# Kernel optimization log

Measured on AMD Instinct MI355X. Metric: run time of the kernel, lower is better.

Reference implementation:

```python
import jax, jax.numpy as jnp
import numpy as np

LR_X = 0.1  # learning_rates[0] from init_kwargs
N_SENSORY = 784


def setup_inputs() -> dict:
    key = jax.random.key(0)
    k1, k2 = jax.random.split(key, 2)
    B, N = 256, 4096
    x = jax.random.normal(k1, (B, N), dtype=jnp.float32)
    # w initialized small, as in _reset_params (0.0001 fill + 1e-4 noise, masked by adj)
    w = jax.random.normal(k2, (N, N), dtype=jnp.float32) * 0.01
    # 1 = node whose value is updated (internal + supervised), 0 = clamped sensory node
    update_mask = jnp.concatenate(
        [jnp.zeros(N_SENSORY, jnp.int32), jnp.ones(N - N_SENSORY, jnp.int32)])
    return {"x": x, "w": w, "update_mask": update_mask, "T": 32}


def reference(x, w, update_mask, T):
    # vanZwol_AMB iterative predictive-coding inference, f = tanh
    m = update_mask.astype(x.dtype)  # [N], 1 = free node

    def f(v):
        return jnp.tanh(v)

    def dfdx(v):
        return 1.0 - jnp.tanh(v) ** 2

    def step(xs, _):
        mu = f(xs) @ w.T                      # [B,N] prediction
        e = (xs - mu) * m                     # use_input_error=False: zero sensory errors
        dEdx = e - dfdx(xs) * (e @ w)         # grad_x (vanZwol_AMB)
        xs = xs - LR_X * m * dEdx             # only internal/supervised nodes updated
        return xs, None

    x, _ = jax.lax.scan(step, x, None, length=T)
    return x
```

## Files before the change

kernel.cpp:

```cpp
#include <hip/hip_runtime.h>
#include <stdint.h>
#include <stddef.h>


#define N_DIM 4096
#define B_DIM 256
#define T_STEPS 32
#define LR_X 0.1f
#define N0 768
#define N_LIVE 3328
#define NCHL 52
#define KG 4
#define KITG 13

typedef unsigned short ushort_t;
using bf16x8 = __attribute__((ext_vector_type(8))) __bf16;
using f32x4  = __attribute__((ext_vector_type(4))) float;

__device__ __forceinline__ ushort_t f2bf(float f) {
    union { float f; unsigned int u; } v; v.f = f;
    unsigned int r = v.u + 0x7fffu + ((v.u >> 16) & 1u);
    return (ushort_t)(r >> 16);
}
__device__ __forceinline__ float bf2f(ushort_t h) {
    union { unsigned int u; float f; } v; v.u = ((unsigned int)h) << 16;
    return v.f;
}

__device__ __forceinline__ int pkidx(int r, int c) {
    const int s = ((r >> 4) << 1) | ((c >> 5) & 1);
    return s * 512 + (r & 15) * 8 + (((c >> 3) & 3) << 7) + (c & 7);
}

__device__ __forceinline__ void async_copy16(const ushort_t* g, ushort_t* l) {
    __builtin_amdgcn_global_load_lds(
        (__attribute__((address_space(1))) void*)(g),
        (__attribute__((address_space(3))) void*)(l),
        16, 0, 0);
}

__global__ __launch_bounds__(256) void pack_w(const float* __restrict__ w,
                                              ushort_t* __restrict__ wpk,
                                              ushort_t* __restrict__ wtpk) {
    __shared__ float tile[64][68];
    const int tid = threadIdx.x;
    const int bid = blockIdx.x;
    int row0, col0; ushort_t* dst; bool tr;
    if (bid < 52 * 64) {
        tr   = false;
        dst  = wpk + (size_t)bid * 4096;
        row0 = N0 + (bid >> 6) * 64;
        col0 = (bid & 63) * 64;
    } else {
        const int b2 = bid - 52 * 64;
        tr   = true;
        dst  = wtpk + (size_t)b2 * 4096;
        const int ntile = b2 / 52, chunk = b2 - ntile * 52;
        row0 = N0 + chunk * 64;
        col0 = N0 + ntile * 64;
    }
    const int rr = tid >> 2, c0 = (tid & 3) * 16;
    const float* src = w + (size_t)(row0 + rr) * N_DIM + col0 + c0;
#pragma unroll
    for (int i = 0; i < 16; i += 4)
        *(float4*)&tile[rr][c0 + i] = *(const float4*)(src + i);
    __syncthreads();
    ushort_t loc[16];
#pragma unroll
    for (int i = 0; i < 16; ++i) {
        const int p = tid * 16 + i;
        const int s = p >> 9, e = p & 511;
        const int r = ((s >> 1) << 4) | ((e >> 3) & 15);
        const int c = ((s & 1) << 5) | (((e >> 7) & 3) << 3) | (e & 7);
        loc[i] = f2bf(tr ? tile[c][r] : tile[r][c]);
    }
    *(uint4*)&dst[tid * 16]     = *(uint4*)&loc[0];
    *(uint4*)&dst[tid * 16 + 8] = *(uint4*)&loc[8];
}

__global__ __launch_bounds__(256) void pack_t_init(const float* __restrict__ xin,
                                                   float* __restrict__ xout,
                                                   ushort_t* __restrict__ tpk) {
    __shared__ float tile[64][68];
    const int tid  = threadIdx.x;
    const int bid  = blockIdx.x;
    const int row0 = (bid >> 6) * 64;
    const int col0 = (bid & 63) * 64;
    const int rr = tid >> 2, c0 = (tid & 3) * 16;
    const size_t sidx = (size_t)(row0 + rr) * N_DIM + col0 + c0;
#pragma unroll
    for (int i = 0; i < 16; i += 4) {
        float4 v = *(const float4*)(xin + sidx + i);
        *(float4*)(xout + sidx + i) = v;
        tile[rr][c0 + i + 0] = tanhf(v.x);
        tile[rr][c0 + i + 1] = tanhf(v.y);
        tile[rr][c0 + i + 2] = tanhf(v.z);
        tile[rr][c0 + i + 3] = tanhf(v.w);
    }
    __syncthreads();
    ushort_t loc[16];
    ushort_t* dst = tpk + (size_t)bid * 4096;
#pragma unroll
    for (int i = 0; i < 16; ++i) {
        const int p = tid * 16 + i;
        const int s = p >> 9, e = p & 511;
        const int r = ((s >> 1) << 4) | ((e >> 3) & 15);
        const int c = ((s & 1) << 5) | (((e >> 7) & 3) << 3) | (e & 7);
        loc[i] = f2bf(tile[r][c]);
    }
    *(uint4*)&dst[tid * 16]     = *(uint4*)&loc[0];
    *(uint4*)&dst[tid * 16 + 8] = *(uint4*)&loc[8];
}

__global__ __launch_bounds__(256) void gemm_mu0(const ushort_t* __restrict__ Apk,
                                                const ushort_t* __restrict__ Bpk,
                                                float* __restrict__ mu0) {
    __shared__ __align__(16) ushort_t As[2][4096];
    __shared__ __align__(16) ushort_t Bs[2][4096];
    const int tid  = threadIdx.x;
    const int lane = tid & 63;
    const int wid  = tid >> 6;
    const int wave_m = wid >> 1, wave_n = wid & 1;
    const int ntile = blockIdx.x, mtile = blockIdx.y;

    const ushort_t* Ab = Apk + (size_t)mtile * 64 * 4096;
    const ushort_t* Bb = Bpk + (size_t)ntile * 64 * 4096;

    auto stage = [&](int buf, int kt) {
#pragma unroll
        for (int u = 0; u < 2; ++u) {
            const int off = (wid * 2 + u) * 512 + lane * 8;
            async_copy16(Ab + (size_t)kt * 4096 + off, &As[buf][off]);
            async_copy16(Bb + (size_t)kt * 4096 + off, &Bs[buf][off]);
        }
    };
    f32x4 acc[2][2] = {};
    auto compute = [&](int buf) {
#pragma unroll
        for (int ks = 0; ks < 2; ++ks) {
            bf16x8 a[2], b[2];
#pragma unroll
            for (int i = 0; i < 2; ++i) {
                const int asub = (wave_m * 2 + i) * 2 + ks;
                const int bsub = (wave_n * 2 + i) * 2 + ks;
                a[i] = *(const bf16x8*)(&As[buf][asub * 512 + lane * 8]);
                b[i] = *(const bf16x8*)(&Bs[buf][bsub * 512 + lane * 8]);
            }
#pragma unroll
            for (int i = 0; i < 2; ++i)
#pragma unroll
                for (int j = 0; j < 2; ++j)
                    acc[i][j] = __builtin_amdgcn_mfma_f32_16x16x32_bf16(
                        a[i], b[j], acc[i][j], 0, 0, 0);
        }
    };
    stage(0, 0);
    __syncthreads();
    for (int kt = 0; kt < 12; ++kt) {
        if (kt + 1 < 12) stage((kt + 1) & 1, kt + 1);
        compute(kt & 1);
        __syncthreads();
    }
    const int l15 = lane & 15, quad = lane >> 4;
#pragma unroll
    for (int j = 0; j < 2; ++j) {
        const int nl = ntile * 64 + wave_n * 32 + j * 16 + l15;
#pragma unroll
        for (int i = 0; i < 2; ++i)
#pragma unroll
            for (int r = 0; r < 4; ++r) {
                const int m = mtile * 64 + wave_m * 32 + i * 16 + quad * 4 + r;
                mu0[(size_t)m * N_LIVE + nl] = acc[i][j][r];
            }
    }
}

template <int SA, int SB, int CO, int PHASE>
__global__ __launch_bounds__(1024) void gemm_fused(
    const ushort_t* __restrict__ Apk,
    const ushort_t* __restrict__ Bpk,
    float* __restrict__ xbuf,
    const float* __restrict__ mu0,
    const int* __restrict__ mask,
    ushort_t* __restrict__ epk,
    ushort_t* __restrict__ tpk) {
    __shared__ __align__(16) ushort_t smem[65536];
    ushort_t* As = smem;
    ushort_t* Bs = smem + 32768;

    const int bid = blockIdx.x;
    const int xcd = bid & 7;
    const int i   = bid >> 3;
    const int nloc = (xcd < 4) ? 7 : 6;
    if (i >= nloc * 4) return;
    const int n0    = (xcd < 4) ? xcd * 7 : 28 + (xcd - 4) * 6;
    const int ntile = n0 + (i >> 2);
    const int mtile = i & 3;

    const int tid  = threadIdx.x;
    const int lane = tid & 63;
    const int g    = tid >> 8;
    const int gtid = tid & 255;
    const int gw   = (tid >> 6) & 3;
    const int wave_m = gw >> 1, wave_n = gw & 1;

    const ushort_t* Ab = Apk + ((size_t)mtile * SA + CO + g * KITG) * 4096;
    const ushort_t* Bb = Bpk + ((size_t)ntile * SB + CO + g * KITG) * 4096;

    auto stage = [&](int buf, int kt) {
        const ushort_t* Ac = Ab + (size_t)kt * 4096;
        const ushort_t* Bc = Bb + (size_t)kt * 4096;
#pragma unroll
        for (int u = 0; u < 2; ++u) {
            const int off = (u * 256 + gtid) * 8;
            async_copy16(Ac + off, &As[(g * 2 + buf) * 4096 + off]);
            async_copy16(Bc + off, &Bs[(g * 2 + buf) * 4096 + off]);
        }
    };

    f32x4 acc[2][2] = {};

    auto compute = [&](int buf) {
#pragma unroll
        for (int ks = 0; ks < 2; ++ks) {
            bf16x8 a[2], b[2];
#pragma unroll
            for (int i2 = 0; i2 < 2; ++i2) {
                const int asub = (wave_m * 2 + i2) * 2 + ks;
                const int bsub = (wave_n * 2 + i2) * 2 + ks;
                a[i2] = *(const bf16x8*)(&As[(g * 2 + buf) * 4096 + asub * 512 + lane * 8]);
                b[i2] = *(const bf16x8*)(&Bs[(g * 2 + buf) * 4096 + bsub * 512 + lane * 8]);
            }
#pragma unroll
            for (int i2 = 0; i2 < 2; ++i2)
#pragma unroll
                for (int j = 0; j < 2; ++j)
                    acc[i2][j] = __builtin_amdgcn_mfma_f32_16x16x32_bf16(
                        a[i2], b[j], acc[i2][j], 0, 0, 0);
        }
    };

    stage(0, 0);
    for (int kt = 0; kt < KITG; ++kt) {
        if (kt + 1 < KITG) {
            stage((kt + 1) & 1, kt + 1);
            asm volatile("s_waitcnt vmcnt(4)" ::: "memory");
        } else {
            asm volatile("s_waitcnt vmcnt(0)" ::: "memory");
        }
        __builtin_amdgcn_s_barrier();
        __builtin_amdgcn_sched_barrier(0);
        compute(kt & 1);
        __builtin_amdgcn_s_barrier();
    }
    __syncthreads();

    float* red = (float*)smem;
    const int RP = 64 * 68;
    {
        const int l15 = lane & 15, quad = lane >> 4;
#pragma unroll
        for (int j = 0; j < 2; ++j) {
            const int col = wave_n * 32 + j * 16 + l15;
#pragma unroll
            for (int i2 = 0; i2 < 2; ++i2)
#pragma unroll
                for (int r = 0; r < 4; ++r) {
                    const int row = wave_m * 32 + i2 * 16 + quad * 4 + r;
                    red[g * RP + row * 68 + col] = acc[i2][j][r];
                }
        }
    }
    __syncthreads();

    const int p4 = tid * 4;
    const int s  = p4 >> 9, e9 = p4 & 511;
    const int r  = ((s >> 1) << 4) | ((e9 >> 3) & 15);
    const int c  = ((s & 1) << 5) | (((e9 >> 7) & 3) << 3) | (e9 & 7);

    float4 sv = *(const float4*)&red[0 * RP + r * 68 + c];
#pragma unroll
    for (int gg = 1; gg < KG; ++gg) {
        float4 v = *(const float4*)&red[gg * RP + r * 68 + c];
        sv.x += v.x; sv.y += v.y; sv.z += v.z; sv.w += v.w;
    }

    const int grow = mtile * 64 + r;
    const int gcl  = ntile * 64 + c;
    const size_t xi = (size_t)grow * N_DIM + N0 + gcl;
    float4 xv = *(const float4*)&xbuf[xi];
    int4   mk = *(const int4*)&mask[N0 + gcl];

    if (PHASE == 1) {
        float4 m0 = *(const float4*)&mu0[(size_t)grow * N_LIVE + gcl];
        ushort_t ev[4];
        ev[0] = f2bf((xv.x - (m0.x + sv.x)) * (float)mk.x);
        ev[1] = f2bf((xv.y - (m0.y + sv.y)) * (float)mk.y);
        ev[2] = f2bf((xv.z - (m0.z + sv.z)) * (float)mk.z);
        ev[3] = f2bf((xv.w - (m0.w + sv.w)) * (float)mk.w);
        *(uint2*)&epk[((size_t)(mtile * NCHL + ntile)) * 4096 + p4]
            = *(uint2*)&ev[0];
    } else {
        const ushort_t* ech = Apk + ((size_t)(mtile * SA + ntile)) * 4096;
        ushort_t ein[4];
        *(uint2*)&ein[0] = *(const uint2*)&ech[p4];
        float xn[4]; ushort_t tv[4];
        const float* svp = &sv.x;
        const int*   mkp = &mk.x;
        const float* xvp = &xv.x;
#pragma unroll
        for (int q = 0; q < 4; ++q) {
            const float x  = xvp[q];
            const float th = tanhf(x);
            const float ee = bf2f(ein[q]);
            xn[q] = x - LR_X * (float)mkp[q] * (ee - (1.0f - th * th) * svp[q]);
            tv[q] = f2bf(tanhf(xn[q]));
        }
        *(float4*)&xbuf[xi] = make_float4(xn[0], xn[1], xn[2], xn[3]);
        *(uint2*)&tpk[((size_t)(mtile * 64 + 12 + ntile)) * 4096 + p4]
            = *(uint2*)&tv[0];
    }
}

extern "C" void kernel_launch(void* const* d_in, const int* in_sizes, int n_in,
                              void* d_out, int out_size, void* d_ws, size_t ws_size,
                              hipStream_t stream) {
    const float* x_in  = (const float*)d_in[0];
    const float* w_in  = (const float*)d_in[1];
    const int*   mask  = (const int*)d_in[2];
    float*       xbuf  = (float*)d_out;

    uint8_t* ws = (uint8_t*)d_ws;
    ushort_t* w_pk  = (ushort_t*)(ws);
    ushort_t* wt_pk = (ushort_t*)(ws + 27262976);
    ushort_t* t_pk  = (ushort_t*)(ws + 49414144);
    ushort_t* e_pk  = (ushort_t*)(ws + 51511296);
    float*    mu0   = (float*)(ws + 53215232);

    pack_w<<<dim3(52 * 64 + 52 * 52), 256, 0, stream>>>(w_in, w_pk, wt_pk);
    pack_t_init<<<dim3(4 * 64), 256, 0, stream>>>(x_in, xbuf, t_pk);
    gemm_mu0<<<dim3(52, 4), 256, 0, stream>>>(t_pk, w_pk, mu0);

    for (int t = 0; t < T_STEPS; ++t) {
        gemm_fused<64, 64, 12, 1><<<256, 1024, 0, stream>>>(
            t_pk, w_pk, xbuf, mu0, mask, e_pk, t_pk);
        gemm_fused<52, 52, 0, 2><<<256, 1024, 0, stream>>>(
            e_pk, wt_pk, xbuf, mu0, mask, e_pk, t_pk);
    }
}
```

Baseline: 1.032 ms.

## Fuse all time steps into one persistent kernel with grid barriers

Replaces the 64 per-step kernel launches with a single persistent kernel that loops over all T steps and synchronises the 208 active blocks with an atomic grid barrier between the two GEMM phases. Each block keeps its x tile, mask and mu0 values in registers across steps, and reuses the fp32 error instead of reloading the bf16 copy. This removes launch gaps and repeated global loads, but relies on all blocks being co-resident and adds spin-wait barrier latency.

```diff
diff --git a/kernel.cpp b/kernel.cpp
--- a/kernel.cpp
+++ b/kernel.cpp
@@ -12,6 +12,7 @@
 #define NCHL 52
 #define KG 4
 #define KITG 13
+#define NB_ACTIVE 208
 
 typedef unsigned short ushort_t;
 using bf16x8 = __attribute__((ext_vector_type(8))) __bf16;
@@ -25,11 +26,6 @@
 __device__ __forceinline__ float bf2f(ushort_t h) {
     union { unsigned int u; float f; } v; v.u = ((unsigned int)h) << 16;
     return v.f;
-}
-
-__device__ __forceinline__ int pkidx(int r, int c) {
-    const int s = ((r >> 4) << 1) | ((c >> 5) & 1);
-    return s * 512 + (r & 15) * 8 + (((c >> 3) & 3) << 7) + (c & 7);
 }
 
 __device__ __forceinline__ void async_copy16(const ushort_t* g, ushort_t* l) {
@@ -175,15 +171,40 @@
     }
 }
 
-template <int SA, int SB, int CO, int PHASE>
-__global__ __launch_bounds__(1024) void gemm_fused(
-    const ushort_t* __restrict__ Apk,
-    const ushort_t* __restrict__ Bpk,
+__global__ void bar_init(unsigned* bar) { bar[0] = 0u; bar[1] = 0u; }
+
+__device__ __forceinline__ void grid_bar(unsigned* bar) {
+    __syncthreads();
+    if (threadIdx.x == 0) {
+        __threadfence();
+        unsigned g = __hip_atomic_load(&bar[1], __ATOMIC_RELAXED,
+                                       __HIP_MEMORY_SCOPE_AGENT);
+        unsigned v = __hip_atomic_fetch_add(&bar[0], 1u, __ATOMIC_ACQ_REL,
+                                            __HIP_MEMORY_SCOPE_AGENT);
+        if (v == NB_ACTIVE - 1) {
+            __hip_atomic_store(&bar[0], 0u, __ATOMIC_RELAXED,
+                               __HIP_MEMORY_SCOPE_AGENT);
+            __hip_atomic_fetch_add(&bar[1], 1u, __ATOMIC_RELEASE,
+                                   __HIP_MEMORY_SCOPE_AGENT);
+        } else {
+            while (__hip_atomic_load(&bar[1], __ATOMIC_ACQUIRE,
+                                     __HIP_MEMORY_SCOPE_AGENT) == g)
+                __builtin_amdgcn_s_sleep(2);
+        }
+        __threadfence();
+    }
+    __syncthreads();
+}
+
+__global__ __launch_bounds__(1024) void pc_persist(
+    const ushort_t* __restrict__ w_pk,
+    const ushort_t* __restrict__ wt_pk,
+    ushort_t* __restrict__ t_pk,
+    ushort_t* __restrict__ e_pk,
     float* __restrict__ xbuf,
     const float* __restrict__ mu0,
     const int* __restrict__ mask,
-    ushort_t* __restrict__ epk,
-    ushort_t* __restrict__ tpk) {
+    unsigned* __restrict__ bar) {
     __shared__ __align__(16) ushort_t smem[65536];
     ushort_t* As = smem;
     ushort_t* Bs = smem + 32768;
@@ -203,62 +224,75 @@
     const int gtid = tid & 255;
     const int gw   = (tid >> 6) & 3;
     const int wave_m = gw >> 1, wave_n = gw & 1;
-
-    const ushort_t* Ab = Apk + ((size_t)mtile * SA + CO + g * KITG) * 4096;
-    const ushort_t* Bb = Bpk + ((size_t)ntile * SB + CO + g * KITG) * 4096;
-
-    auto stage = [&](int buf, int kt) {
-        const ushort_t* Ac = Ab + (size_t)kt * 4096;
-        const ushort_t* Bc = Bb + (size_t)kt * 4096;
-#pragma unroll
-        for (int u = 0; u < 2; ++u) {
-            const int off = (u * 256 + gtid) * 8;
-            async_copy16(Ac + off, &As[(g * 2 + buf) * 4096 + off]);
-            async_copy16(Bc + off, &Bs[(g * 2 + buf) * 4096 + off]);
-        }
-    };
-
-    f32x4 acc[2][2] = {};
-
-    auto compute = [&](int buf) {
-#pragma unroll
-        for (int ks = 0; ks < 2; ++ks) {
-            bf16x8 a[2], b[2];
-#pragma unroll
-            for (int i2 = 0; i2 < 2; ++i2) {
-                const int asub = (wave_m * 2 + i2) * 2 + ks;
-                const int bsub = (wave_n * 2 + i2) * 2 + ks;
-                a[i2] = *(const bf16x8*)(&As[(g * 2 + buf) * 4096 + asub * 512 + lane * 8]);
-                b[i2] = *(const bf16x8*)(&Bs[(g * 2 + buf) * 4096 + bsub * 512 + lane * 8]);
-            }
-#pragma unroll
-            for (int i2 = 0; i2 < 2; ++i2)
-#pragma unroll
-                for (int j = 0; j < 2; ++j)
-                    acc[i2][j] = __builtin_amdgcn_mfma_f32_16x16x32_bf16(
-                        a[i2], b[j], acc[i2][j], 0, 0, 0);
-        }
-    };
-
-    stage(0, 0);
-    for (int kt = 0; kt < KITG; ++kt) {
-        if (kt + 1 < KITG) {
-            stage((kt + 1) & 1, kt + 1);
-            asm volatile("s_waitcnt vmcnt(4)" ::: "memory");
-        } else {
-            asm volatile("s_waitcnt vmcnt(0)" ::: "memory");
-        }
-        __builtin_amdgcn_s_barrier();
-        __builtin_amdgcn_sched_barrier(0);
-        compute(kt & 1);
-        __builtin_amdgcn_s_barrier();
-    }
-    __syncthreads();
+    const int l15 = lane & 15, quad = lane >> 4;
+
+    ushort_t* Asg = As + g * 2 * 4096;
+    ushort_t* Bsg = Bs + g * 2 * 4096;
+
+    const int p4 = tid * 4;
+    const int s  = p4 >> 9, e9 = p4 & 511;
+    const int rr = ((s >> 1) << 4) | ((e9 >> 3) & 15);
+    const int cc = ((s & 1) << 5) | (((e9 >> 7) & 3) << 3) | (e9 & 7);
+    const int grow = mtile * 64 + rr;
+    const int gcl  = ntile * 64 + cc;
+    const size_t xi = (size_t)grow * N_DIM + N0 + gcl;
 
     float* red = (float*)smem;
     const int RP = 64 * 68;
-    {
-        const int l15 = lane & 15, quad = lane >> 4;
+
+    float4 xv = *(const float4*)&xbuf[xi];
+    const int4   mk = *(const int4*)&mask[N0 + gcl];
+    const float4 m0 = *(const float4*)&mu0[(size_t)grow * N_LIVE + gcl];
+    float em[4];
+
+    auto run_panel = [&](const ushort_t* Ab, const ushort_t* Bb,
+                         f32x4 (&acc)[2][2]) {
+        auto stage = [&](int buf, int kt) {
+            const ushort_t* Ac = Ab + (size_t)kt * 4096;
+            const ushort_t* Bc = Bb + (size_t)kt * 4096;
+#pragma unroll
+            for (int u = 0; u < 2; ++u) {
+                const int off = (u * 256 + gtid) * 8;
+                async_copy16(Ac + off, &Asg[buf * 4096 + off]);
+                async_copy16(Bc + off, &Bsg[buf * 4096 + off]);
+            }
+        };
+        auto compute = [&](int buf) {
+#pragma unroll
+            for (int ks = 0; ks < 2; ++ks) {
+                bf16x8 a[2], b[2];
+#pragma unroll
+                for (int i2 = 0; i2 < 2; ++i2) {
+                    const int asub = (wave_m * 2 + i2) * 2 + ks;
+                    const int bsub = (wave_n * 2 + i2) * 2 + ks;
+                    a[i2] = *(const bf16x8*)(&Asg[buf * 4096 + asub * 512 + lane * 8]);
+                    b[i2] = *(const bf16x8*)(&Bsg[buf * 4096 + bsub * 512 + lane * 8]);
+                }
+#pragma unroll
+                for (int i2 = 0; i2 < 2; ++i2)
+#pragma unroll
+                    for (int j = 0; j < 2; ++j)
+                        acc[i2][j] = __builtin_amdgcn_mfma_f32_16x16x32_bf16(
+                            a[i2], b[j], acc[i2][j], 0, 0, 0);
+            }
+        };
+        stage(0, 0);
+        for (int kt = 0; kt < KITG; ++kt) {
+            if (kt + 1 < KITG) {
+                stage((kt + 1) & 1, kt + 1);
+                asm volatile("s_waitcnt vmcnt(4)" ::: "memory");
+            } else {
+                asm volatile("s_waitcnt vmcnt(0)" ::: "memory");
+            }
+            __builtin_amdgcn_s_barrier();
+            __builtin_amdgcn_sched_barrier(0);
+            compute(kt & 1);
+            __builtin_amdgcn_s_barrier();
+        }
+    };
+
+    auto reduce_sum = [&](f32x4 (&acc)[2][2]) -> float4 {
+        __syncthreads();
 #pragma unroll
         for (int j = 0; j < 2; ++j) {
             const int col = wave_n * 32 + j * 16 + l15;
@@ -270,56 +304,57 @@
                     red[g * RP + row * 68 + col] = acc[i2][j][r];
                 }
         }
-    }
-    __syncthreads();
-
-    const int p4 = tid * 4;
-    const int s  = p4 >> 9, e9 = p4 & 511;
-    const int r  = ((s >> 1) << 4) | ((e9 >> 3) & 15);
-    const int c  = ((s & 1) << 5) | (((e9 >> 7) & 3) << 3) | (e9 & 7);
-
-    float4 sv = *(const float4*)&red[0 * RP + r * 68 + c];
-#pragma unroll
-    for (int gg = 1; gg < KG; ++gg) {
-        float4 v = *(const float4*)&red[gg * RP + r * 68 + c];
-        sv.x += v.x; sv.y += v.y; sv.z += v.z; sv.w += v.w;
-    }
-
-    const int grow = mtile * 64 + r;
-    const int gcl  = ntile * 64 + c;
-    const size_t xi = (size_t)grow * N_DIM + N0 + gcl;
-    float4 xv = *(const float4*)&xbuf[xi];
-    int4   mk = *(const int4*)&mask[N0 + gcl];
-
-    if (PHASE == 1) {
-        float4 m0 = *(const float4*)&mu0[(size_t)grow * N_LIVE + gcl];
-        ushort_t ev[4];
-        ev[0] = f2bf((xv.x - (m0.x + sv.x)) * (float)mk.x);
-        ev[1] = f2bf((xv.y - (m0.y + sv.y)) * (float)mk.y);
-        ev[2] = f2bf((xv.z - (m0.z + sv.z)) * (float)mk.z);
-        ev[3] = f2bf((xv.w - (m0.w + sv.w)) * (float)mk.w);
-        *(uint2*)&epk[((size_t)(mtile * NCHL + ntile)) * 4096 + p4]
-            = *(uint2*)&ev[0];
-    } else {
-        const ushort_t* ech = Apk + ((size_t)(mtile * SA + ntile)) * 4096;
-        ushort_t ein[4];
-        *(uint2*)&ein[0] = *(const uint2*)&ech[p4];
-        float xn[4]; ushort_t tv[4];
-        const float* svp = &sv.x;
-        const int*   mkp = &mk.x;
-        const float* xvp = &xv.x;
-#pragma unroll
-        for (int q = 0; q < 4; ++q) {
-            const float x  = xvp[q];
-            const float th = tanhf(x);
-            const float ee = bf2f(ein[q]);
-            xn[q] = x - LR_X * (float)mkp[q] * (ee - (1.0f - th * th) * svp[q]);
-            tv[q] = f2bf(tanhf(xn[q]));
-        }
-        *(float4*)&xbuf[xi] = make_float4(xn[0], xn[1], xn[2], xn[3]);
-        *(uint2*)&tpk[((size_t)(mtile * 64 + 12 + ntile)) * 4096 + p4]
-            = *(uint2*)&tv[0];
-    }
+        __syncthreads();
+        float4 sv = *(const float4*)&red[0 * RP + rr * 68 + cc];
+#pragma unroll
+        for (int gg = 1; gg < KG; ++gg) {
+            float4 v = *(const float4*)&red[gg * RP + rr * 68 + cc];
+            sv.x += v.x; sv.y += v.y; sv.z += v.z; sv.w += v.w;
+        }
+        return sv;
+    };
+
+    const ushort_t* Ab1 = t_pk + ((size_t)(mtile * 64 + 12 + g * KITG)) * 4096;
+    const ushort_t* Bb1 = w_pk + ((size_t)(ntile * 64 + 12 + g * KITG)) * 4096;
+    const ushort_t* Ab2 = e_pk + ((size_t)(mtile * NCHL + g * KITG)) * 4096;
+    const ushort_t* Bb2 = wt_pk + ((size_t)(ntile * NCHL + g * KITG)) * 4096;
+    ushort_t* eout = e_pk + ((size_t)(mtile * NCHL + ntile)) * 4096 + p4;
+    ushort_t* tout = t_pk + ((size_t)(mtile * 64 + 12 + ntile)) * 4096 + p4;
+
+    for (int t = 0; t < T_STEPS; ++t) {
+        {
+            f32x4 acc[2][2] = {};
+            run_panel(Ab1, Bb1, acc);
+            float4 sv = reduce_sum(acc);
+            em[0] = (xv.x - (m0.x + sv.x)) * (float)mk.x;
+            em[1] = (xv.y - (m0.y + sv.y)) * (float)mk.y;
+            em[2] = (xv.z - (m0.z + sv.z)) * (float)mk.z;
+            em[3] = (xv.w - (m0.w + sv.w)) * (float)mk.w;
+            ushort_t ev[4] = { f2bf(em[0]), f2bf(em[1]), f2bf(em[2]), f2bf(em[3]) };
+            *(uint2*)eout = *(uint2*)&ev[0];
+        }
+        grid_bar(bar);
+        {
+            f32x4 acc[2][2] = {};
+            run_panel(Ab2, Bb2, acc);
+            float4 sv = reduce_sum(acc);
+            float* xp = &xv.x;
+            const float* svp = &sv.x;
+            const int* mkp = &mk.x;
+            ushort_t tv[4];
+#pragma unroll
+            for (int q = 0; q < 4; ++q) {
+                const float x  = xp[q];
+                const float th = tanhf(x);
+                xp[q] = x - LR_X * (float)mkp[q]
+                            * (em[q] - (1.0f - th * th) * svp[q]);
+                tv[q] = f2bf(tanhf(xp[q]));
+            }
+            *(uint2*)tout = *(uint2*)&tv[0];
+        }
+        grid_bar(bar);
+    }
+    *(float4*)&xbuf[xi] = xv;
 }
 
 extern "C" void kernel_launch(void* const* d_in, const int* in_sizes, int n_in,
@@ -336,15 +371,13 @@
     ushort_t* t_pk  = (ushort_t*)(ws + 49414144);
     ushort_t* e_pk  = (ushort_t*)(ws + 51511296);
     float*    mu0   = (float*)(ws + 53215232);
+    unsigned* bar   = (unsigned*)(ws + 56623104);
 
     pack_w<<<dim3(52 * 64 + 52 * 52), 256, 0, stream>>>(w_in, w_pk, wt_pk);
     pack_t_init<<<dim3(4 * 64), 256, 0, stream>>>(x_in, xbuf, t_pk);
     gemm_mu0<<<dim3(52, 4), 256, 0, stream>>>(t_pk, w_pk, mu0);
-
-    for (int t = 0; t < T_STEPS; ++t) {
-        gemm_fused<64, 64, 12, 1><<<256, 1024, 0, stream>>>(
-            t_pk, w_pk, xbuf, mu0, mask, e_pk, t_pk);
-        gemm_fused<52, 52, 0, 2><<<256, 1024, 0, stream>>>(
-            e_pk, wt_pk, xbuf, mu0, mask, e_pk, t_pk);
-    }
-}
+    bar_init<<<1, 1, 0, stream>>>(bar);
+
+    pc_persist<<<256, 1024, 0, stream>>>(
+        w_pk, wt_pk, t_pk, e_pk, xbuf, mu0, mask, bar);
+}
```

Measured after the change: 3.447 ms. 234% more time.

## Store live weight blocks as scaled FP8 e4m3 and expand to bf16 in-kernel

Applied to the files above, without the earlier changes.

Packs the live-node weight blocks (both W and W^T) into FP8 e4m3 with a fixed scale of 256, keeping only the sensory columns in bf16 for the initial mu0 GEMM. The per-step fused GEMMs stream half as many weight bytes and convert FP8 to bf16 with bit manipulation before the bf16 MFMA. This targets the memory traffic of re-reading the weight matrix each iteration. It adds ALU work for conversion and loses precision, and the fixed scale assumes small-magnitude weights.

```diff
diff --git a/kernel.cpp b/kernel.cpp
--- a/kernel.cpp
+++ b/kernel.cpp
@@ -27,37 +27,68 @@
     return v.f;
 }
 
-__device__ __forceinline__ int pkidx(int r, int c) {
-    const int s = ((r >> 4) << 1) | ((c >> 5) & 1);
-    return s * 512 + (r & 15) * 8 + (((c >> 3) & 3) << 7) + (c & 7);
-}
-
-__device__ __forceinline__ void async_copy16(const ushort_t* g, ushort_t* l) {
+__device__ __forceinline__ unsigned char f2e4m3_s8(float f) {
+    f *= 256.0f;
+    union { float f; unsigned int u; } v; v.f = f;
+    const unsigned s = (v.u >> 24) & 0x80u;
+    const unsigned absu = v.u & 0x7FFFFFFFu;
+    const unsigned r = absu + 0x7FFFFu + ((absu >> 20) & 1u);
+    const int e4 = (int)((r >> 23) & 0xFF) - 120;
+    const unsigned m3 = (r >> 20) & 7u;
+    if (e4 <= 0)  return (unsigned char)s;
+    if (e4 > 15)  return (unsigned char)(s | 0x7E);
+    return (unsigned char)(s | ((unsigned)e4 << 3) | m3);
+}
+
+__device__ __forceinline__ bf16x8 fp8x8_to_bf16x8(uint2 d) {
+    union { unsigned u[4]; bf16x8 v; } o;
+    unsigned x = d.x;
+    o.u[0] = ((((x & 0x80u) << 8) | ((x & 0x8000u) << 16)
+             | ((x & 0x7Fu) << 4) | ((x & 0x7F00u) << 12)) + 0x38003800u);
+    x >>= 16;
+    o.u[1] = ((((x & 0x80u) << 8) | ((x & 0x8000u) << 16)
+             | ((x & 0x7Fu) << 4) | ((x & 0x7F00u) << 12)) + 0x38003800u);
+    unsigned y = d.y;
+    o.u[2] = ((((y & 0x80u) << 8) | ((y & 0x8000u) << 16)
+             | ((y & 0x7Fu) << 4) | ((y & 0x7F00u) << 12)) + 0x38003800u);
+    y >>= 16;
+    o.u[3] = ((((y & 0x80u) << 8) | ((y & 0x8000u) << 16)
+             | ((y & 0x7Fu) << 4) | ((y & 0x7F00u) << 12)) + 0x38003800u);
+    return o.v;
+}
+
+__device__ __forceinline__ void async_copy16(const void* g, void* l) {
     __builtin_amdgcn_global_load_lds(
-        (__attribute__((address_space(1))) void*)(g),
+        (__attribute__((address_space(1))) const void*)(g),
         (__attribute__((address_space(3))) void*)(l),
         16, 0, 0);
 }
 
 __global__ __launch_bounds__(256) void pack_w(const float* __restrict__ w,
-                                              ushort_t* __restrict__ wpk,
-                                              ushort_t* __restrict__ wtpk) {
+                                              ushort_t* __restrict__ wsen,
+                                              uint8_t* __restrict__ wl8,
+                                              uint8_t* __restrict__ wt8) {
     __shared__ float tile[64][68];
     const int tid = threadIdx.x;
     const int bid = blockIdx.x;
-    int row0, col0; ushort_t* dst; bool tr;
-    if (bid < 52 * 64) {
-        tr   = false;
-        dst  = wpk + (size_t)bid * 4096;
-        row0 = N0 + (bid >> 6) * 64;
-        col0 = (bid & 63) * 64;
+    int row0, col0; bool tr, f8; ushort_t* dst16 = nullptr; uint8_t* dst8 = nullptr;
+    if (bid < 624) {
+        tr = false; f8 = false;
+        const int ntile = bid / 12, ch = bid - ntile * 12;
+        row0 = N0 + ntile * 64; col0 = ch * 64;
+        dst16 = wsen + (size_t)bid * 4096;
+    } else if (bid < 3328) {
+        tr = false; f8 = true;
+        const int b2 = bid - 624;
+        const int ntile = b2 / 52, cl = b2 - ntile * 52;
+        row0 = N0 + ntile * 64; col0 = N0 + cl * 64;
+        dst8 = wl8 + (size_t)b2 * 4096;
     } else {
-        const int b2 = bid - 52 * 64;
-        tr   = true;
-        dst  = wtpk + (size_t)b2 * 4096;
-        const int ntile = b2 / 52, chunk = b2 - ntile * 52;
-        row0 = N0 + chunk * 64;
-        col0 = N0 + ntile * 64;
+        tr = true; f8 = true;
+        const int b3 = bid - 3328;
+        const int ntile = b3 / 52, cl = b3 - ntile * 52;
+        row0 = N0 + cl * 64; col0 = N0 + ntile * 64;
+        dst8 = wt8 + (size_t)b3 * 4096;
     }
     const int rr = tid >> 2, c0 = (tid & 3) * 16;
     const float* src = w + (size_t)(row0 + rr) * N_DIM + col0 + c0;
@@ -65,17 +96,30 @@
     for (int i = 0; i < 16; i += 4)
         *(float4*)&tile[rr][c0 + i] = *(const float4*)(src + i);
     __syncthreads();
-    ushort_t loc[16];
-#pragma unroll
-    for (int i = 0; i < 16; ++i) {
-        const int p = tid * 16 + i;
-        const int s = p >> 9, e = p & 511;
-        const int r = ((s >> 1) << 4) | ((e >> 3) & 15);
-        const int c = ((s & 1) << 5) | (((e >> 7) & 3) << 3) | (e & 7);
-        loc[i] = f2bf(tr ? tile[c][r] : tile[r][c]);
-    }
-    *(uint4*)&dst[tid * 16]     = *(uint4*)&loc[0];
-    *(uint4*)&dst[tid * 16 + 8] = *(uint4*)&loc[8];
+    if (!f8) {
+        ushort_t loc[16];
+#pragma unroll
+        for (int i = 0; i < 16; ++i) {
+            const int p = tid * 16 + i;
+            const int s = p >> 9, e = p & 511;
+            const int r = ((s >> 1) << 4) | ((e >> 3) & 15);
+            const int c = ((s & 1) << 5) | (((e >> 7) & 3) << 3) | (e & 7);
+            loc[i] = f2bf(tile[r][c]);
+        }
+        *(uint4*)&dst16[tid * 16]     = *(uint4*)&loc[0];
+        *(uint4*)&dst16[tid * 16 + 8] = *(uint4*)&loc[8];
+    } else {
+        unsigned char loc[16];
+#pragma unroll
+        for (int i = 0; i < 16; ++i) {
+            const int p = tid * 16 + i;
+            const int s = p >> 9, e = p & 511;
+            const int r = ((s >> 1) << 4) | ((e >> 3) & 15);
+            const int c = ((s & 1) << 5) | (((e >> 7) & 3) << 3) | (e & 7);
+            loc[i] = f2e4m3_s8(tr ? tile[c][r] : tile[r][c]);
+        }
+        *(uint4*)&dst8[tid * 16] = *(uint4*)&loc[0];
+    }
 }
 
 __global__ __launch_bounds__(256) void pack_t_init(const float* __restrict__ xin,
@@ -113,7 +157,7 @@
 }
 
 __global__ __launch_bounds__(256) void gemm_mu0(const ushort_t* __restrict__ Apk,
-                                                const ushort_t* __restrict__ Bpk,
+                                                const ushort_t* __restrict__ wsen,
                                                 float* __restrict__ mu0) {
     __shared__ __align__(16) ushort_t As[2][4096];
     __shared__ __align__(16) ushort_t Bs[2][4096];
@@ -124,7 +168,7 @@
     const int ntile = blockIdx.x, mtile = blockIdx.y;
 
     const ushort_t* Ab = Apk + (size_t)mtile * 64 * 4096;
-    const ushort_t* Bb = Bpk + (size_t)ntile * 64 * 4096;
+    const ushort_t* Bb = wsen + (size_t)ntile * 12 * 4096;
 
     auto stage = [&](int buf, int kt) {
 #pragma unroll
@@ -175,18 +219,18 @@
     }
 }
 
-template <int SA, int SB, int CO, int PHASE>
+template <int SA, int CO, int PHASE>
 __global__ __launch_bounds__(1024) void gemm_fused(
     const ushort_t* __restrict__ Apk,
-    const ushort_t* __restrict__ Bpk,
+    const uint8_t* __restrict__ Bpk8,
     float* __restrict__ xbuf,
     const float* __restrict__ mu0,
     const int* __restrict__ mask,
     ushort_t* __restrict__ epk,
     ushort_t* __restrict__ tpk) {
-    __shared__ __align__(16) ushort_t smem[65536];
-    ushort_t* As = smem;
-    ushort_t* Bs = smem + 32768;
+    __shared__ __align__(16) uint8_t smem[98304];
+    ushort_t* As  = (ushort_t*)smem;
+    uint8_t*  Bs8 = smem + 65536;
 
     const int bid = blockIdx.x;
     const int xcd = bid & 7;
@@ -205,17 +249,20 @@
     const int wave_m = gw >> 1, wave_n = gw & 1;
 
     const ushort_t* Ab = Apk + ((size_t)mtile * SA + CO + g * KITG) * 4096;
-    const ushort_t* Bb = Bpk + ((size_t)ntile * SB + CO + g * KITG) * 4096;
+    const uint8_t*  Bb = Bpk8 + ((size_t)ntile * NCHL + g * KITG) * 4096;
+
+    ushort_t* Asg = As + g * 2 * 4096;
+    uint8_t*  Bsg = Bs8 + g * 2 * 4096;
 
     auto stage = [&](int buf, int kt) {
         const ushort_t* Ac = Ab + (size_t)kt * 4096;
-        const ushort_t* Bc = Bb + (size_t)kt * 4096;
+        const uint8_t*  Bc = Bb + (size_t)kt * 4096;
 #pragma unroll
         for (int u = 0; u < 2; ++u) {
             const int off = (u * 256 + gtid) * 8;
-            async_copy16(Ac + off, &As[(g * 2 + buf) * 4096 + off]);
-            async_copy16(Bc + off, &Bs[(g * 2 + buf) * 4096 + off]);
-        }
+            async_copy16(Ac + off, &Asg[buf * 4096 + off]);
+        }
+        async_copy16(Bc + gtid * 16, &Bsg[buf * 4096 + gtid * 16]);
     };
 
     f32x4 acc[2][2] = {};
@@ -228,8 +275,9 @@
             for (int i2 = 0; i2 < 2; ++i2) {
                 const int asub = (wave_m * 2 + i2) * 2 + ks;
                 const int bsub = (wave_n * 2 + i2) * 2 + ks;
-                a[i2] = *(const bf16x8*)(&As[(g * 2 + buf) * 4096 + asub * 512 + lane * 8]);
-                b[i2] = *(const bf16x8*)(&Bs[(g * 2 + buf) * 4096 + bsub * 512 + lane * 8]);
+                a[i2] = *(const bf16x8*)(&Asg[buf * 4096 + asub * 512 + lane * 8]);
+                b[i2] = fp8x8_to_bf16x8(
+                    *(const uint2*)(&Bsg[buf * 4096 + bsub * 512 + lane * 8]));
             }
 #pragma unroll
             for (int i2 = 0; i2 < 2; ++i2)
@@ -244,7 +292,7 @@
     for (int kt = 0; kt < KITG; ++kt) {
         if (kt + 1 < KITG) {
             stage((kt + 1) & 1, kt + 1);
-            asm volatile("s_waitcnt vmcnt(4)" ::: "memory");
+            asm volatile("s_waitcnt vmcnt(3)" ::: "memory");
         } else {
             asm volatile("s_waitcnt vmcnt(0)" ::: "memory");
         }
@@ -331,20 +379,21 @@
     float*       xbuf  = (float*)d_out;
 
     uint8_t* ws = (uint8_t*)d_ws;
-    ushort_t* w_pk  = (ushort_t*)(ws);
-    ushort_t* wt_pk = (ushort_t*)(ws + 27262976);
-    ushort_t* t_pk  = (ushort_t*)(ws + 49414144);
-    ushort_t* e_pk  = (ushort_t*)(ws + 51511296);
-    float*    mu0   = (float*)(ws + 53215232);
-
-    pack_w<<<dim3(52 * 64 + 52 * 52), 256, 0, stream>>>(w_in, w_pk, wt_pk);
+    ushort_t* w_sen = (ushort_t*)(ws);
+    uint8_t*  w_l8  = (uint8_t*)(ws + 5111808);
+    uint8_t*  wt_8  = (uint8_t*)(ws + 16187392);
+    ushort_t* t_pk  = (ushort_t*)(ws + 27262976);
+    ushort_t* e_pk  = (ushort_t*)(ws + 29360128);
+    float*    mu0   = (float*)(ws + 31064064);
+
+    pack_w<<<dim3(6032), 256, 0, stream>>>(w_in, w_sen, w_l8, wt_8);
     pack_t_init<<<dim3(4 * 64), 256, 0, stream>>>(x_in, xbuf, t_pk);
-    gemm_mu0<<<dim3(52, 4), 256, 0, stream>>>(t_pk, w_pk, mu0);
+    gemm_mu0<<<dim3(52, 4), 256, 0, stream>>>(t_pk, w_sen, mu0);
 
     for (int t = 0; t < T_STEPS; ++t) {
-        gemm_fused<64, 64, 12, 1><<<256, 1024, 0, stream>>>(
-            t_pk, w_pk, xbuf, mu0, mask, e_pk, t_pk);
-        gemm_fused<52, 52, 0, 2><<<256, 1024, 0, stream>>>(
-            e_pk, wt_pk, xbuf, mu0, mask, e_pk, t_pk);
-    }
-}
+        gemm_fused<64, 12, 1><<<256, 1024, 0, stream>>>(
+            t_pk, w_l8, xbuf, mu0, mask, e_pk, t_pk);
+        gemm_fused<52, 0, 2><<<256, 1024, 0, stream>>>(
+            e_pk, wt_8, xbuf, mu0, mask, e_pk, t_pk);
+    }
+}
```

After: 1.895 ms. +83.6%, slower.
